# Optimization experiments

Measured on AMD Instinct MI355X. Metric: run time of the kernel, lower is better.

The kernel has to match this reference:

```python
import jax, jax.numpy as jnp
import numpy as np

L = 10                      # layers
DIL = [2 ** l for l in range(L)]  # dilations, kernel_size = 2
C = 128                     # residual channels
CS = 256                    # skip channels
V = 256                     # q_levels / vocab
B = 32                      # batch of decode streams
RF = 1 + sum(DIL)           # receptive field = 1024


def setup_inputs() -> dict:
    key = jax.random.key(0)
    ks = jax.random.split(key, 16)
    s = 1.0 / np.sqrt(C)
    inp = {
        "prompt": jax.random.randint(ks[0], (B, RF), 0, V, dtype=jnp.int32),
        "n_steps": 512,
        "E": jax.random.normal(ks[1], (V, C), jnp.float32) * 0.1,
        "Wf": jax.random.normal(ks[2], (L, C, C, 2), jnp.float32) * s,
        "Wg": jax.random.normal(ks[3], (L, C, C, 2), jnp.float32) * s,
        "bf": jnp.zeros((L, C), jnp.float32),
        "bg": jnp.zeros((L, C), jnp.float32),
        "Wres": jax.random.normal(ks[4], (L, C, C), jnp.float32) * s,
        "bres": jnp.zeros((L, C), jnp.float32),
        "Wskip": jax.random.normal(ks[5], (L, C, CS), jnp.float32) * s,
        "bskip": jnp.zeros((L, CS), jnp.float32),
        "Wo1": jax.random.normal(ks[6], (CS, CS), jnp.float32) / np.sqrt(CS),
        "bo1": jnp.zeros((CS,), jnp.float32),
        "Wo2": jax.random.normal(ks[7], (CS, V), jnp.float32) / np.sqrt(CS),
        "bo2": jnp.zeros((V,), jnp.float32),
    }
    return inp


def reference(prompt, n_steps, E, Wf, Wg, bf, bg, Wres, bres,
              Wskip, bskip, Wo1, bo1, Wo2, bo2):
    # ---- teacher-forced pass over the prompt: fills per-layer queues ----
    def head(skips):
        h = jax.nn.relu(skips)
        h = jax.nn.relu(h @ Wo1 + bo1)
        return h @ Wo2 + bo2

    x = E[prompt]                              # [B, T, C]
    skips = jnp.zeros((), jnp.float32)
    layer_ins = []                             # input to each residual layer
    T = prompt.shape[1]
    for l, d in enumerate(DIL):
        layer_ins.append(x)
        xd = jnp.pad(x, ((0, 0), (d, 0), (0, 0)))[:, :T]   # causal shift by d
        f = jnp.tanh(xd @ Wf[l, ..., 0] + x @ Wf[l, ..., 1] + bf[l])
        g = jax.nn.sigmoid(xd @ Wg[l, ..., 0] + x @ Wg[l, ..., 1] + bg[l])
        z = f * g
        skips = skips + z @ Wskip[l] + bskip[l]
        x = x + z @ Wres[l] + bres[l]
    logits = head(skips)                       # [B, T, V]
    tok0 = jnp.argmax(logits[:, -1], axis=-1).astype(prompt.dtype)  # first prediction
    # per-layer rolling queue: last d_l inputs to layer l (ring buffer)
    bufs = tuple(layer_ins[l][:, -DIL[l]:, :] for l in range(L))

    # ---- single-sample decode loop (rolling-queue fast generation) ----
    def step(carry, _):
        tok, bufs = carry
        x = E[tok]                             # [B, C]
        skips = jnp.zeros((), jnp.float32)
        new_bufs = []
        for l in range(L):
            past = bufs[l][:, 0, :]            # x_{t - d_l}
            f = jnp.tanh(past @ Wf[l, ..., 0] + x @ Wf[l, ..., 1] + bf[l])
            g = jax.nn.sigmoid(past @ Wg[l, ..., 0] + x @ Wg[l, ..., 1] + bg[l])
            z = f * g
            skips = skips + z @ Wskip[l] + bskip[l]
            # roll queue and push this layer's current input
            new_bufs.append(jnp.roll(bufs[l], -1, axis=1).at[:, -1, :].set(x))
            x = x + z @ Wres[l] + bres[l]
        nxt = jnp.argmax(head(skips), axis=-1).astype(tok.dtype)
        return (nxt, tuple(new_bufs)), tok

    (_, _), toks = jax.lax.scan(step, (tok0, bufs), None, length=n_steps)
    return jnp.concatenate([prompt, toks.T], axis=1)   # [B, T + n_steps]
```

## Files before the change

### kernel.cpp

```cpp
#include <hip/hip_runtime.h>
#include <math.h>

#define NL 10
#define C 128
#define CS 256
#define NV 256
#define NB 32
#define TT 1024
#define WPC 8
#define NTHR 256
#define CH_STRIDE 8192

__device__ __forceinline__ float atomLoadF(const float* p) {
  return __hip_atomic_load(p, __ATOMIC_RELAXED, __HIP_MEMORY_SCOPE_AGENT);
}
__device__ __forceinline__ void atomStoreF(float* p, float v) {
  __hip_atomic_store(p, v, __ATOMIC_RELAXED, __HIP_MEMORY_SCOPE_AGENT);
}
__device__ __forceinline__ unsigned atomLoadU(const unsigned* p) {
  return __hip_atomic_load(p, __ATOMIC_RELAXED, __HIP_MEMORY_SCOPE_AGENT);
}
__device__ __forceinline__ void atomStoreU(unsigned* p, unsigned v) {
  __hip_atomic_store(p, v, __ATOMIC_RELAXED, __HIP_MEMORY_SCOPE_AGENT);
}

__device__ __forceinline__ void chainbar(unsigned* ctr, unsigned& target) {
  target += WPC;
  asm volatile("s_waitcnt vmcnt(0) lgkmcnt(0)" ::: "memory");
  __syncthreads();
  if (threadIdx.x == 0) {
    __hip_atomic_fetch_add(ctr, 1u, __ATOMIC_RELAXED, __HIP_MEMORY_SCOPE_AGENT);
    while (__hip_atomic_load(ctr, __ATOMIC_RELAXED, __HIP_MEMORY_SCOPE_AGENT) < target) {}
  }
  __syncthreads();
  asm volatile("" ::: "memory");
}

__global__ __launch_bounds__(256) void k_embed(const int* __restrict__ prompt,
                                               const float* __restrict__ E,
                                               float* __restrict__ X) {
  int idx = blockIdx.x * 256 + threadIdx.x;
  const float4* E4 = (const float4*)E;
  float4* X4 = (float4*)X;
#pragma unroll
  for (int p = 0; p < 4; ++p) {
    int i = idx + p * 262144;
    int row = i >> 5, c4 = i & 31;
    int tk = prompt[row];
    X4[i] = E4[tk * 32 + c4];
  }
}

__global__ __launch_bounds__(256) void k_layer(
    const float* __restrict__ Xin, float* __restrict__ Xout,
    const float* __restrict__ Wf, const float* __restrict__ Wg,
    const float* __restrict__ bf, const float* __restrict__ bg,
    const float* __restrict__ Wres, const float* __restrict__ bres,
    float* __restrict__ rings, float* __restrict__ zlast, int l) {
  const int tid = threadIdx.x;
  const int m = blockIdx.x;
  const int b = m >> 3;
  const int t0 = (m & 7) << 7;
  const int d = 1 << l;

  __shared__ __align__(16) float sm[12416];
  float* Axd = sm;
  float* Ax  = sm + 16 * 132;
  float* Wfs = sm + 32 * 132;
  float* Wgs = Wfs + 16 * 256;

  const int rg = tid >> 4, cg = tid & 15;

  float af[8][8] = {};
  float ag[8][8] = {};

  for (int kc = 0; kc < 8; ++kc) {
    __syncthreads();
#pragma unroll
    for (int p = 0; p < 2; ++p) {
      int li = tid + p * 256;
      int row = li >> 2, c4 = li & 3;
      int ci = kc * 16 + c4 * 4;
      int t = t0 + row;
      float4 vx = *(const float4*)(Xin + ((size_t)b * TT + t) * C + ci);
      float4 vd = make_float4(0.f, 0.f, 0.f, 0.f);
      int ts = t - d;
      if (ts >= 0) vd = *(const float4*)(Xin + ((size_t)b * TT + ts) * C + ci);
      Ax[(c4 * 4 + 0) * 132 + row] = vx.x;
      Ax[(c4 * 4 + 1) * 132 + row] = vx.y;
      Ax[(c4 * 4 + 2) * 132 + row] = vx.z;
      Ax[(c4 * 4 + 3) * 132 + row] = vx.w;
      Axd[(c4 * 4 + 0) * 132 + row] = vd.x;
      Axd[(c4 * 4 + 1) * 132 + row] = vd.y;
      Axd[(c4 * 4 + 2) * 132 + row] = vd.z;
      Axd[(c4 * 4 + 3) * 132 + row] = vd.w;
    }
#pragma unroll
    for (int p = 0; p < 4; ++p) {
      int li = tid + p * 256;
      int ci = li >> 6, cc = (li & 63) << 2;
      size_t off = ((size_t)(l * C + kc * 16 + ci) * C) * 2 + cc;
      *(float4*)&Wfs[ci * 256 + cc] = *(const float4*)(Wf + off);
      *(float4*)&Wgs[ci * 256 + cc] = *(const float4*)(Wg + off);
    }
    __syncthreads();
    for (int ci = 0; ci < 16; ++ci) {
      float4 d0 = *(float4*)&Axd[ci * 132 + rg * 8];
      float4 d1 = *(float4*)&Axd[ci * 132 + rg * 8 + 4];
      float4 x0 = *(float4*)&Ax[ci * 132 + rg * 8];
      float4 x1 = *(float4*)&Ax[ci * 132 + rg * 8 + 4];
      float axd[8] = {d0.x, d0.y, d0.z, d0.w, d1.x, d1.y, d1.z, d1.w};
      float ax[8]  = {x0.x, x0.y, x0.z, x0.w, x1.x, x1.y, x1.z, x1.w};
#pragma unroll
      for (int jj = 0; jj < 4; ++jj) {
        float4 wf = *(float4*)&Wfs[ci * 256 + cg * 16 + jj * 4];
        float4 wg = *(float4*)&Wgs[ci * 256 + cg * 16 + jj * 4];
#pragma unroll
        for (int i = 0; i < 8; ++i) {
          af[i][2 * jj]     += axd[i] * wf.x + ax[i] * wf.y;
          af[i][2 * jj + 1] += axd[i] * wf.z + ax[i] * wf.w;
          ag[i][2 * jj]     += axd[i] * wg.x + ax[i] * wg.y;
          ag[i][2 * jj + 1] += axd[i] * wg.z + ax[i] * wg.w;
        }
      }
    }
  }

  float bfv[8], bgv[8];
#pragma unroll
  for (int j = 0; j < 8; ++j) {
    bfv[j] = bf[l * C + cg * 8 + j];
    bgv[j] = bg[l * C + cg * 8 + j];
  }
#pragma unroll
  for (int i = 0; i < 8; ++i)
#pragma unroll
    for (int j = 0; j < 8; ++j) {
      float fv = tanhf(af[i][j] + bfv[j]);
      float gv = 1.f / (1.f + expf(-(ag[i][j] + bgv[j])));
      af[i][j] = fv * gv;
    }
  if (((m & 7) == 7) && rg == 15) {
#pragma unroll
    for (int j = 0; j < 8; ++j)
      zlast[((size_t)l * NB + b) * C + cg * 8 + j] = af[7][j];
  }
#pragma unroll
  for (int i = 0; i < 8; ++i)
#pragma unroll
    for (int j = 0; j < 8; ++j) ag[i][j] = 0.f;

  float* zs  = sm;
  float* Wrs = sm + 32 * 132;
  for (int c = 0; c < 4; ++c) {
    __syncthreads();
    if ((cg >> 2) == c) {
      int kl = (cg & 3) * 8;
#pragma unroll
      for (int i = 0; i < 8; ++i)
#pragma unroll
        for (int j = 0; j < 8; ++j) zs[(kl + j) * 132 + rg * 8 + i] = af[i][j];
    }
#pragma unroll
    for (int p = 0; p < 4; ++p) {
      int li = tid + p * 256;
      int kr = li >> 5, cc = (li & 31) << 2;
      *(float4*)&Wrs[kr * 128 + cc] =
          *(const float4*)(Wres + ((size_t)(l * C + c * 32 + kr)) * C + cc);
    }
    __syncthreads();
    for (int k = 0; k < 32; ++k) {
      float4 a0 = *(float4*)&zs[k * 132 + rg * 8];
      float4 a1 = *(float4*)&zs[k * 132 + rg * 8 + 4];
      float4 w0 = *(float4*)&Wrs[k * 128 + cg * 8];
      float4 w1 = *(float4*)&Wrs[k * 128 + cg * 8 + 4];
      float a[8] = {a0.x, a0.y, a0.z, a0.w, a1.x, a1.y, a1.z, a1.w};
      float wv[8] = {w0.x, w0.y, w0.z, w0.w, w1.x, w1.y, w1.z, w1.w};
#pragma unroll
      for (int i = 0; i < 8; ++i)
#pragma unroll
        for (int j = 0; j < 8; ++j) ag[i][j] += a[i] * wv[j];
    }
  }

  float brv[8];
#pragma unroll
  for (int j = 0; j < 8; ++j) brv[j] = bres[l * C + cg * 8 + j];
#pragma unroll
  for (int i = 0; i < 8; ++i) {
    int t = t0 + rg * 8 + i;
    const float4* xi = (const float4*)(Xin + ((size_t)b * TT + t) * C + cg * 8);
    float4 v0 = xi[0], v1 = xi[1];
    float o[8] = {v0.x, v0.y, v0.z, v0.w, v1.x, v1.y, v1.z, v1.w};
#pragma unroll
    for (int j = 0; j < 8; ++j) o[j] += brv[j] + ag[i][j];
    float4* xo = (float4*)(Xout + ((size_t)b * TT + t) * C + cg * 8);
    xo[0] = make_float4(o[0], o[1], o[2], o[3]);
    xo[1] = make_float4(o[4], o[5], o[6], o[7]);
    if (t >= TT - d) {
      int slot = t - (TT - d);
      float* rp = rings + (size_t)(d - 1) * NB * C + ((size_t)slot * NB + b) * C + cg * 8;
      *(float4*)&rp[0] = v0;
      *(float4*)&rp[4] = v1;
    }
  }
}

__global__ __launch_bounds__(256) void k_head0(
    const float* __restrict__ zlast, const float* __restrict__ Wskip,
    const float* __restrict__ bskip, const float* __restrict__ Wo1,
    const float* __restrict__ bo1, const float* __restrict__ Wo2,
    const float* __restrict__ bo2, float* __restrict__ chst,
    int* __restrict__ dout, int ostride) {
  int b = blockIdx.x, tid = threadIdx.x;
  __shared__ float zl[NL][C];
  __shared__ float sr[CS];
  __shared__ float h1[CS];
  __shared__ float lg[NV];
#pragma unroll
  for (int p = 0; p < 5; ++p) {
    int li = tid + p * 256;
    zl[li >> 7][li & 127] = zlast[((size_t)(li >> 7) * NB + b) * C + (li & 127)];
  }
  __syncthreads();
  float s = 0.f;
  for (int l = 0; l < NL; ++l) {
    s += bskip[l * CS + tid];
    const float* wp = Wskip + (size_t)(l * C) * CS + tid;
    for (int k = 0; k < C; ++k) s += zl[l][k] * wp[(size_t)k * CS];
  }
  sr[tid] = fmaxf(s, 0.f);
  __syncthreads();
  float h = bo1[tid];
  {
    const float* wp = Wo1 + tid;
    for (int k = 0; k < CS; ++k) h += sr[k] * wp[(size_t)k * CS];
  }
  h1[tid] = fmaxf(h, 0.f);
  __syncthreads();
  float lv = bo2[tid];
  {
    const float* wp = Wo2 + tid;
    for (int k = 0; k < CS; ++k) lv += h1[k] * wp[(size_t)k * NV];
  }
  lg[tid] = lv;
  __syncthreads();
  if (tid == 0) {
    float bv = lg[0]; int bi = 0;
    for (int v = 1; v < NV; ++v)
      if (lg[v] > bv) { bv = lg[v]; bi = v; }
    ((unsigned*)(chst + (size_t)b * CH_STRIDE))[16] = (unsigned)bi;
    dout[(size_t)b * ostride + TT] = bi;
  }
}

__global__ __launch_bounds__(256) void k_copyprompt(const int* __restrict__ prompt,
                                                    int* __restrict__ dout,
                                                    int ostride) {
  int idx = blockIdx.x * 256 + threadIdx.x;
  int b = idx >> 10, t = idx & 1023;
  dout[(size_t)b * ostride + t] = prompt[idx];
}

__global__ __launch_bounds__(NTHR) void k_decode(
    const float* __restrict__ E, const float* __restrict__ Wf,
    const float* __restrict__ Wg, const float* __restrict__ bf,
    const float* __restrict__ bg, const float* __restrict__ Wres,
    const float* __restrict__ bres, const float* __restrict__ Wskip,
    const float* __restrict__ bskip, const float* __restrict__ Wo1,
    const float* __restrict__ bo1, const float* __restrict__ Wo2,
    const float* __restrict__ bo2, float* __restrict__ rings,
    float* __restrict__ chst, int* __restrict__ dout, int ostride) {
  const int tid = threadIdx.x;
  const int chain = blockIdx.x & 31;
  const int w = blockIdx.x >> 5;
  const int nsteps = ostride - TT;

  float* st = chst + (size_t)chain * CH_STRIDE;
  unsigned* ctr = (unsigned*)st;
  float* xpart = st + 64;
  float* skipp = st + 2176;
  float* h1g   = st + 4224;
  float* pmaxg = st + 4480;
  unsigned* pidxg = (unsigned*)(st + 4488);

  __shared__ float past[NL][C];
  __shared__ float xx[C];
  __shared__ float zbuf[16];
  __shared__ float fred[16][17];
  __shared__ float gred[16][17];
  __shared__ float skipr[CS];
  __shared__ float h1f[CS];
  __shared__ float hred[32][9];
  __shared__ float lgt[32];
  __shared__ float bsum[CS];
  __shared__ unsigned toksh;

  {
    float s = 0.f;
    for (int l = 0; l < NL; ++l) s += bskip[l * CS + tid];
    bsum[tid] = s;
  }
  __syncthreads();
  unsigned tok = ((const unsigned*)st)[16];
  unsigned target = 0;

  const int col = tid & 15, kg = tid >> 4;
  const int hj = tid & 31, hkg = tid >> 5;

  for (int s = 0; s < nsteps - 1; ++s) {
    if (tid < C) xx[tid] = E[(size_t)tok * C + tid];
#pragma unroll
    for (int p = 0; p < 5; ++p) {
      int li = tid + p * NTHR;
      int lp = li >> 7, cc = li & 127;
      int dd = 1 << lp;
      int slot = s & (dd - 1);
      past[lp][cc] = atomLoadF(
          &rings[(size_t)(dd - 1) * NB * C + (size_t)slot * NB * C + chain * C + cc]);
    }
    float skip_acc = 0.f;
    __syncthreads();

    for (int l = 0; l < NL; ++l) {
      const float* wfp = Wf + ((size_t)(l * C) * C + (w * 16 + col)) * 2;
      const float* wgp = Wg + ((size_t)(l * C) * C + (w * 16 + col)) * 2;
      float pf = 0.f, pg = 0.f;
#pragma unroll
      for (int i = 0; i < 8; ++i) {
        int ci = kg + 16 * i;
        float2 wf2 = *(const float2*)(wfp + (size_t)ci * C * 2);
        float2 wg2 = *(const float2*)(wgp + (size_t)ci * C * 2);
        float pv = past[l][ci], xv = xx[ci];
        pf += pv * wf2.x + xv * wf2.y;
        pg += pv * wg2.x + xv * wg2.y;
      }
      fred[col][kg] = pf;
      gred[col][kg] = pg;
      __syncthreads();
      if (tid < 16) {
        float sf = 0.f, sg = 0.f;
#pragma unroll
        for (int k = 0; k < 16; ++k) { sf += fred[tid][k]; sg += gred[tid][k]; }
        sf += bf[l * C + w * 16 + tid];
        sg += bg[l * C + w * 16 + tid];
        zbuf[tid] = tanhf(sf) * (1.f / (1.f + expf(-sg)));
      }
      __syncthreads();
      {
        const float* wsp = Wskip + (size_t)(l * C + w * 16) * CS + tid;
        float a = 0.f;
#pragma unroll
        for (int j = 0; j < 16; ++j) a += zbuf[j] * wsp[(size_t)j * CS];
        skip_acc += a;
      }
      if (l < NL - 1) {
        float oldx = 0.f;
        if (tid < C) {
          const float* wrp = Wres + (size_t)(l * C + w * 16) * C + tid;
          float a = 0.f;
#pragma unroll
          for (int j = 0; j < 16; ++j) a += zbuf[j] * wrp[(size_t)j * C];
          atomStoreF(&xpart[((l & 1) * 8 + w) * C + tid], a);
          oldx = xx[tid];
        }
        chainbar(ctr, target);
        if (tid < C) {
          float nx = xx[tid] + bres[l * C + tid];
#pragma unroll
          for (int wi = 0; wi < 8; ++wi)
            nx += atomLoadF(&xpart[((l & 1) * 8 + wi) * C + tid]);
          if (w == 0) {
            int dd = 1 << l, slot = s & (dd - 1);
            atomStoreF(&rings[(size_t)(dd - 1) * NB * C + (size_t)slot * NB * C +
                              chain * C + tid],
                       oldx);
          }
          xx[tid] = nx;
        }
        __syncthreads();
      } else {
        if (w == 0 && tid < C) {
          int dd = 1 << l, slot = s & (dd - 1);
          atomStoreF(&rings[(size_t)(dd - 1) * NB * C + (size_t)slot * NB * C +
                            chain * C + tid],
                     xx[tid]);
        }
      }
    }

    atomStoreF(&skipp[w * CS + tid], skip_acc);
    chainbar(ctr, target);
    {
      float sk = bsum[tid];
#pragma unroll
      for (int wi = 0; wi < 8; ++wi) sk += atomLoadF(&skipp[wi * CS + tid]);
      skipr[tid] = fmaxf(sk, 0.f);
    }
    __syncthreads();
    {
      const float* wp = Wo1 + w * 32 + hj;
      float a = 0.f;
      for (int k = hkg * 32; k < hkg * 32 + 32; ++k) a += skipr[k] * wp[(size_t)k * CS];
      hred[hj][hkg] = a;
      __syncthreads();
      if (tid < 32) {
        float v = 0.f;
#pragma unroll
        for (int k = 0; k < 8; ++k) v += hred[tid][k];
        v += bo1[w * 32 + tid];
        atomStoreF(&h1g[w * 32 + tid], fmaxf(v, 0.f));
      }
    }
    chainbar(ctr, target);
    h1f[tid] = atomLoadF(&h1g[tid]);
    __syncthreads();
    {
      const float* wp = Wo2 + w * 32 + hj;
      float a = 0.f;
      for (int k = hkg * 32; k < hkg * 32 + 32; ++k) a += h1f[k] * wp[(size_t)k * NV];
      hred[hj][hkg] = a;
      __syncthreads();
      if (tid < 32) {
        float v = 0.f;
#pragma unroll
        for (int k = 0; k < 8; ++k) v += hred[tid][k];
        lgt[tid] = v + bo2[w * 32 + tid];
      }
      __syncthreads();
      if (tid == 0) {
        float bv = lgt[0]; int bi = 0;
        for (int j = 1; j < 32; ++j)
          if (lgt[j] > bv) { bv = lgt[j]; bi = j; }
        atomStoreF(&pmaxg[w], bv);
        atomStoreU(&pidxg[w], (unsigned)(w * 32 + bi));
      }
    }
    chainbar(ctr, target);
    if (tid == 0) {
      float bv = atomLoadF(&pmaxg[0]);
      unsigned bi = atomLoadU(&pidxg[0]);
#pragma unroll
      for (int wi = 1; wi < 8; ++wi) {
        float v = atomLoadF(&pmaxg[wi]);
        if (v > bv) { bv = v; bi = atomLoadU(&pidxg[wi]); }
      }
      toksh = bi;
      if (w == 0) dout[(size_t)chain * ostride + TT + s + 1] = (int)bi;
    }
    __syncthreads();
    tok = toksh;
  }
}

extern "C" void kernel_launch(void* const* d_in, const int* in_sizes, int n_in,
                              void* d_out, int out_size, void* d_ws, size_t ws_size,
                              hipStream_t stream) {
  const int* prompt = (const int*)d_in[0];
  const float* E    = (const float*)d_in[2];
  const float* Wf   = (const float*)d_in[3];
  const float* Wg   = (const float*)d_in[4];
  const float* bf   = (const float*)d_in[5];
  const float* bg   = (const float*)d_in[6];
  const float* Wres = (const float*)d_in[7];
  const float* bres = (const float*)d_in[8];
  const float* Wskip= (const float*)d_in[9];
  const float* bskip= (const float*)d_in[10];
  const float* Wo1  = (const float*)d_in[11];
  const float* bo1  = (const float*)d_in[12];
  const float* Wo2  = (const float*)d_in[13];
  const float* bo2  = (const float*)d_in[14];
  int* dout = (int*)d_out;
  int ostride = out_size / NB;

  float* ws = (float*)d_ws;
  float* X0    = ws;
  float* X1    = ws + 4194304;
  float* rings = ws + 8388608;
  float* zlast = ws + 12578816;
  float* chst  = ws + 12619776;

  hipMemsetAsync(chst, 0, (size_t)NB * CH_STRIDE * sizeof(float), stream);
  k_embed<<<1024, 256, 0, stream>>>(prompt, E, X0);
  float* xa = X0; float* xb = X1;
  for (int l = 0; l < NL; ++l) {
    k_layer<<<256, 256, 0, stream>>>(xa, xb, Wf, Wg, bf, bg, Wres, bres, rings, zlast, l);
    float* t = xa; xa = xb; xb = t;
  }
  k_head0<<<NB, 256, 0, stream>>>(zlast, Wskip, bskip, Wo1, bo1, Wo2, bo2, chst, dout, ostride);
  k_copyprompt<<<128, 256, 0, stream>>>(prompt, dout, ostride);
  k_decode<<<NB * WPC, NTHR, 0, stream>>>(E, Wf, Wg, bf, bg, Wres, bres, Wskip, bskip,
                                          Wo1, bo1, Wo2, bo2, rings, chst, dout, ostride);
}
```

Baseline: 35.18 ms.

## Replace counter barriers with tagged 64-bit flag exchange and register weight prefetch

Cross-block synchronisation in the decode loop stops using a shared atomic counter barrier. Each value now travels as a 64-bit word holding a float and a step tag, and consumers spin until the tags match. Gate, skip, residual and head weights are prefetched into registers one layer ahead, and the past-input half of the gate dot product is computed early. The ring buffer is filled for the next step while the skip reduction is still pending, and biases are cached in shared memory. Storage for rings and exchange buffers doubles, register pressure rises, and per-slot tag spinning adds polling traffic.

```diff
diff --git a/kernel.cpp b/kernel.cpp
--- a/kernel.cpp
+++ b/kernel.cpp
@@ -9,31 +9,21 @@
 #define TT 1024
 #define WPC 8
 #define NTHR 256
-#define CH_STRIDE 8192
-
-__device__ __forceinline__ float atomLoadF(const float* p) {
+#define CH_BYTES 131072
+
+typedef unsigned long long ull;
+
+__device__ __forceinline__ ull aLoad64(const ull* p) {
   return __hip_atomic_load(p, __ATOMIC_RELAXED, __HIP_MEMORY_SCOPE_AGENT);
 }
-__device__ __forceinline__ void atomStoreF(float* p, float v) {
+__device__ __forceinline__ void aStore64(ull* p, ull v) {
   __hip_atomic_store(p, v, __ATOMIC_RELAXED, __HIP_MEMORY_SCOPE_AGENT);
 }
-__device__ __forceinline__ unsigned atomLoadU(const unsigned* p) {
-  return __hip_atomic_load(p, __ATOMIC_RELAXED, __HIP_MEMORY_SCOPE_AGENT);
-}
-__device__ __forceinline__ void atomStoreU(unsigned* p, unsigned v) {
-  __hip_atomic_store(p, v, __ATOMIC_RELAXED, __HIP_MEMORY_SCOPE_AGENT);
-}
-
-__device__ __forceinline__ void chainbar(unsigned* ctr, unsigned& target) {
-  target += WPC;
-  asm volatile("s_waitcnt vmcnt(0) lgkmcnt(0)" ::: "memory");
-  __syncthreads();
-  if (threadIdx.x == 0) {
-    __hip_atomic_fetch_add(ctr, 1u, __ATOMIC_RELAXED, __HIP_MEMORY_SCOPE_AGENT);
-    while (__hip_atomic_load(ctr, __ATOMIC_RELAXED, __HIP_MEMORY_SCOPE_AGENT) < target) {}
-  }
-  __syncthreads();
-  asm volatile("" ::: "memory");
+__device__ __forceinline__ ull packF(float x, unsigned tag) {
+  return ((ull)__float_as_uint(x) << 32) | (ull)tag;
+}
+__device__ __forceinline__ float unpackF(ull v) {
+  return __uint_as_float((unsigned)(v >> 32));
 }
 
 __global__ __launch_bounds__(256) void k_embed(const int* __restrict__ prompt,
@@ -56,7 +46,7 @@
     const float* __restrict__ Wf, const float* __restrict__ Wg,
     const float* __restrict__ bf, const float* __restrict__ bg,
     const float* __restrict__ Wres, const float* __restrict__ bres,
-    float* __restrict__ rings, float* __restrict__ zlast, int l) {
+    ull* __restrict__ rings, float* __restrict__ zlast, int l) {
   const int tid = threadIdx.x;
   const int m = blockIdx.x;
   const int b = m >> 3;
@@ -199,9 +189,10 @@
     xo[1] = make_float4(o[4], o[5], o[6], o[7]);
     if (t >= TT - d) {
       int slot = t - (TT - d);
-      float* rp = rings + (size_t)(d - 1) * NB * C + ((size_t)slot * NB + b) * C + cg * 8;
-      *(float4*)&rp[0] = v0;
-      *(float4*)&rp[4] = v1;
+      ull* rp = rings + (size_t)(d - 1) * NB * C + ((size_t)slot * NB + b) * C + cg * 8;
+      float vin[8] = {v0.x, v0.y, v0.z, v0.w, v1.x, v1.y, v1.z, v1.w};
+#pragma unroll
+      for (int j = 0; j < 8; ++j) rp[j] = packF(vin[j], 0u);
     }
   }
 }
@@ -210,7 +201,7 @@
     const float* __restrict__ zlast, const float* __restrict__ Wskip,
     const float* __restrict__ bskip, const float* __restrict__ Wo1,
     const float* __restrict__ bo1, const float* __restrict__ Wo2,
-    const float* __restrict__ bo2, float* __restrict__ chst,
+    const float* __restrict__ bo2, char* __restrict__ chst,
     int* __restrict__ dout, int ostride) {
   int b = blockIdx.x, tid = threadIdx.x;
   __shared__ float zl[NL][C];
@@ -249,7 +240,7 @@
     float bv = lg[0]; int bi = 0;
     for (int v = 1; v < NV; ++v)
       if (lg[v] > bv) { bv = lg[v]; bi = v; }
-    ((unsigned*)(chst + (size_t)b * CH_STRIDE))[16] = (unsigned)bi;
+    *(unsigned*)(chst + (size_t)b * CH_BYTES) = (unsigned)bi;
     dout[(size_t)b * ostride + TT] = bi;
   }
 }
@@ -262,78 +253,128 @@
   dout[(size_t)b * ostride + t] = prompt[idx];
 }
 
-__global__ __launch_bounds__(NTHR) void k_decode(
+__global__ __launch_bounds__(NTHR, 1) void k_decode(
     const float* __restrict__ E, const float* __restrict__ Wf,
     const float* __restrict__ Wg, const float* __restrict__ bf,
     const float* __restrict__ bg, const float* __restrict__ Wres,
     const float* __restrict__ bres, const float* __restrict__ Wskip,
     const float* __restrict__ bskip, const float* __restrict__ Wo1,
     const float* __restrict__ bo1, const float* __restrict__ Wo2,
-    const float* __restrict__ bo2, float* __restrict__ rings,
-    float* __restrict__ chst, int* __restrict__ dout, int ostride) {
+    const float* __restrict__ bo2, ull* __restrict__ rings,
+    char* __restrict__ chst, int* __restrict__ dout, int ostride) {
   const int tid = threadIdx.x;
   const int chain = blockIdx.x & 31;
   const int w = blockIdx.x >> 5;
   const int nsteps = ostride - TT;
 
-  float* st = chst + (size_t)chain * CH_STRIDE;
-  unsigned* ctr = (unsigned*)st;
-  float* xpart = st + 64;
-  float* skipp = st + 2176;
-  float* h1g   = st + 4224;
-  float* pmaxg = st + 4480;
-  unsigned* pidxg = (unsigned*)(st + 4488);
+  char* cb = chst + (size_t)chain * CH_BYTES;
+  ull* xp  = (ull*)(cb + 1024);
+  ull* skp = (ull*)(cb + 74752);
+  ull* h1p = (ull*)(cb + 91136);
+  ull* amx = (ull*)(cb + 93184);
 
   __shared__ float past[NL][C];
   __shared__ float xx[C];
-  __shared__ float zbuf[16];
   __shared__ float fred[16][17];
   __shared__ float gred[16][17];
+  __shared__ float zbuf[16];
   __shared__ float skipr[CS];
   __shared__ float h1f[CS];
   __shared__ float hred[32][9];
   __shared__ float lgt[32];
+  __shared__ ull am[8];
+  __shared__ float bfl[NL][16], bgl[NL][16];
+  __shared__ float brl[NL - 1][C];
   __shared__ float bsum[CS];
-  __shared__ unsigned toksh;
-
+
+  for (int li = tid; li < NL * 16; li += NTHR) {
+    bfl[li >> 4][li & 15] = bf[(li >> 4) * C + w * 16 + (li & 15)];
+    bgl[li >> 4][li & 15] = bg[(li >> 4) * C + w * 16 + (li & 15)];
+  }
+  for (int li = tid; li < (NL - 1) * C; li += NTHR)
+    brl[li >> 7][li & 127] = bres[(li >> 7) * C + (li & 127)];
   {
-    float s = 0.f;
-    for (int l = 0; l < NL; ++l) s += bskip[l * CS + tid];
-    bsum[tid] = s;
-  }
-  __syncthreads();
-  unsigned tok = ((const unsigned*)st)[16];
-  unsigned target = 0;
+    float sacc = 0.f;
+    for (int l = 0; l < NL; ++l) sacc += bskip[l * CS + tid];
+    bsum[tid] = sacc;
+  }
+
+  unsigned tok = *(const unsigned*)cb;
 
   const int col = tid & 15, kg = tid >> 4;
   const int hj = tid & 31, hkg = tid >> 5;
 
-  for (int s = 0; s < nsteps - 1; ++s) {
-    if (tid < C) xx[tid] = E[(size_t)tok * C + tid];
+  float2 gwf[2][8], gwg[2][8];
+  float wresr[2][16], wskipr[2][16];
+  float pfp[2], pgp[2];
+
+  auto ringLoad = [&](int s2) {
 #pragma unroll
     for (int p = 0; p < 5; ++p) {
       int li = tid + p * NTHR;
       int lp = li >> 7, cc = li & 127;
-      int dd = 1 << lp;
-      int slot = s & (dd - 1);
-      past[lp][cc] = atomLoadF(
-          &rings[(size_t)(dd - 1) * NB * C + (size_t)slot * NB * C + chain * C + cc]);
+      int D = 1 << lp;
+      int slot = s2 & (D - 1);
+      unsigned expv = (s2 >= D) ? (unsigned)(s2 - D + 1) : 0u;
+      const ull* rp =
+          rings + (size_t)(D - 1) * NB * C + ((size_t)slot * NB + chain) * C + cc;
+      ull v = aLoad64(rp);
+      while ((unsigned)v != expv) v = aLoad64(rp);
+      past[lp][cc] = unpackF(v);
+    }
+  };
+  auto gatePrefetch = [&](int l, int buf) {
+#pragma unroll
+    for (int i = 0; i < 8; ++i) {
+      int ci = kg + 16 * i;
+      gwf[buf][i] = *(const float2*)(Wf + ((size_t)(l * C + ci) * C + (w * 16 + col)) * 2);
+      gwg[buf][i] = *(const float2*)(Wg + ((size_t)(l * C + ci) * C + (w * 16 + col)) * 2);
+    }
+#pragma unroll
+    for (int j = 0; j < 16; ++j)
+      wskipr[buf][j] = Wskip[(size_t)(l * C + w * 16 + j) * CS + tid];
+    if (l < NL - 1 && tid < C) {
+#pragma unroll
+      for (int j = 0; j < 16; ++j)
+        wresr[buf][j] = Wres[(size_t)(l * C + w * 16 + j) * C + tid];
+    }
+  };
+  auto pastDot = [&](int l, int buf) {
+    float a = 0.f, bacc = 0.f;
+#pragma unroll
+    for (int i = 0; i < 8; ++i) {
+      float pv = past[l][kg + 16 * i];
+      a += pv * gwf[buf][i].x;
+      bacc += pv * gwg[buf][i].x;
+    }
+    pfp[buf] = a;
+    pgp[buf] = bacc;
+  };
+
+  ringLoad(0);
+  gatePrefetch(0, 0);
+  __syncthreads();
+  pastDot(0, 0);
+
+  for (int s = 0; s < nsteps - 1; ++s) {
+    const unsigned tg = (unsigned)(s + 1);
+    float xreg = 0.f;
+    if (tid < C) {
+      xreg = E[(size_t)tok * C + tid];
+      xx[tid] = xreg;
     }
     float skip_acc = 0.f;
     __syncthreads();
 
+#pragma unroll
     for (int l = 0; l < NL; ++l) {
-      const float* wfp = Wf + ((size_t)(l * C) * C + (w * 16 + col)) * 2;
-      const float* wgp = Wg + ((size_t)(l * C) * C + (w * 16 + col)) * 2;
-      float pf = 0.f, pg = 0.f;
+      const int buf = l & 1, nbuf = buf ^ 1;
+      float pf = pfp[buf], pg = pgp[buf];
 #pragma unroll
       for (int i = 0; i < 8; ++i) {
-        int ci = kg + 16 * i;
-        float2 wf2 = *(const float2*)(wfp + (size_t)ci * C * 2);
-        float2 wg2 = *(const float2*)(wgp + (size_t)ci * C * 2);
-        float pv = past[l][ci], xv = xx[ci];
-        pf += pv * wf2.x + xv * wf2.y;
-        pg += pv * wg2.x + xv * wg2.y;
+        float xv = xx[kg + 16 * i];
+        pf += xv * gwf[buf][i].y;
+        pg += xv * gwg[buf][i].y;
       }
       fred[col][kg] = pf;
       gred[col][kg] = pg;
@@ -342,114 +383,155 @@
         float sf = 0.f, sg = 0.f;
 #pragma unroll
         for (int k = 0; k < 16; ++k) { sf += fred[tid][k]; sg += gred[tid][k]; }
-        sf += bf[l * C + w * 16 + tid];
-        sg += bg[l * C + w * 16 + tid];
-        zbuf[tid] = tanhf(sf) * (1.f / (1.f + expf(-sg)));
+        sf += bfl[l][tid];
+        sg += bgl[l][tid];
+        zbuf[tid] = tanhf(sf) / (1.f + expf(-sg));
       }
       __syncthreads();
-      {
-        const float* wsp = Wskip + (size_t)(l * C + w * 16) * CS + tid;
-        float a = 0.f;
-#pragma unroll
-        for (int j = 0; j < 16; ++j) a += zbuf[j] * wsp[(size_t)j * CS];
-        skip_acc += a;
-      }
+      float oldx = xreg;
       if (l < NL - 1) {
-        float oldx = 0.f;
         if (tid < C) {
-          const float* wrp = Wres + (size_t)(l * C + w * 16) * C + tid;
-          float a = 0.f;
-#pragma unroll
-          for (int j = 0; j < 16; ++j) a += zbuf[j] * wrp[(size_t)j * C];
-          atomStoreF(&xpart[((l & 1) * 8 + w) * C + tid], a);
-          oldx = xx[tid];
+          float part = 0.f;
+#pragma unroll
+          for (int j = 0; j < 16; ++j) part += zbuf[j] * wresr[buf][j];
+          aStore64(&xp[((size_t)l * 8 + w) * C + tid], packF(part, tg));
         }
-        chainbar(ctr, target);
+        gatePrefetch(l + 1, nbuf);
+        {
+          float sa = 0.f;
+#pragma unroll
+          for (int j = 0; j < 16; ++j) sa += zbuf[j] * wskipr[buf][j];
+          skip_acc += sa;
+        }
+        pastDot(l + 1, nbuf);
         if (tid < C) {
-          float nx = xx[tid] + bres[l * C + tid];
-#pragma unroll
-          for (int wi = 0; wi < 8; ++wi)
-            nx += atomLoadF(&xpart[((l & 1) * 8 + wi) * C + tid]);
-          if (w == 0) {
-            int dd = 1 << l, slot = s & (dd - 1);
-            atomStoreF(&rings[(size_t)(dd - 1) * NB * C + (size_t)slot * NB * C +
-                              chain * C + tid],
-                       oldx);
+          const ull* base = &xp[(size_t)l * 8 * C + tid];
+          ull v[8];
+          bool ok;
+          do {
+            ok = true;
+#pragma unroll
+            for (int i2 = 0; i2 < 8; ++i2) v[i2] = aLoad64(base + (size_t)i2 * C);
+#pragma unroll
+            for (int i2 = 0; i2 < 8; ++i2) ok &= ((unsigned)v[i2] == tg);
+          } while (!ok);
+          float xnew = oldx + brl[l][tid];
+#pragma unroll
+          for (int i2 = 0; i2 < 8; ++i2) xnew += unpackF(v[i2]);
+          xreg = xnew;
+          xx[tid] = xnew;
+          if (w == (l & 7)) {
+            int D = 1 << l, slot = s & (D - 1);
+            aStore64(&rings[(size_t)(D - 1) * NB * C + ((size_t)slot * NB + chain) * C + tid],
+                     packF(oldx, tg));
           }
-          xx[tid] = nx;
         }
         __syncthreads();
       } else {
-        if (w == 0 && tid < C) {
-          int dd = 1 << l, slot = s & (dd - 1);
-          atomStoreF(&rings[(size_t)(dd - 1) * NB * C + (size_t)slot * NB * C +
-                            chain * C + tid],
-                     xx[tid]);
+        {
+          float sa = 0.f;
+#pragma unroll
+          for (int j = 0; j < 16; ++j) sa += zbuf[j] * wskipr[buf][j];
+          skip_acc += sa;
+        }
+        if (w == (9 & 7) && tid < C) {
+          int slot = s & 511;
+          aStore64(&rings[(size_t)511 * NB * C + ((size_t)slot * NB + chain) * C + tid],
+                   packF(xreg, tg));
         }
       }
     }
 
-    atomStoreF(&skipp[w * CS + tid], skip_acc);
-    chainbar(ctr, target);
+    aStore64(&skp[(size_t)w * CS + tid], packF(skip_acc, tg));
+    gatePrefetch(0, 0);
+    float wo1r[32];
+#pragma unroll
+    for (int k2 = 0; k2 < 32; ++k2)
+      wo1r[k2] = Wo1[(size_t)(hkg * 32 + k2) * CS + w * 32 + hj];
+    ringLoad(s + 1);
     {
+      const ull* base = &skp[tid];
+      ull v[8];
+      bool ok;
+      do {
+        ok = true;
+#pragma unroll
+        for (int i2 = 0; i2 < 8; ++i2) v[i2] = aLoad64(base + (size_t)i2 * CS);
+#pragma unroll
+        for (int i2 = 0; i2 < 8; ++i2) ok &= ((unsigned)v[i2] == tg);
+      } while (!ok);
       float sk = bsum[tid];
 #pragma unroll
-      for (int wi = 0; wi < 8; ++wi) sk += atomLoadF(&skipp[wi * CS + tid]);
+      for (int i2 = 0; i2 < 8; ++i2) sk += unpackF(v[i2]);
       skipr[tid] = fmaxf(sk, 0.f);
     }
     __syncthreads();
+    pastDot(0, 0);
     {
-      const float* wp = Wo1 + w * 32 + hj;
       float a = 0.f;
-      for (int k = hkg * 32; k < hkg * 32 + 32; ++k) a += skipr[k] * wp[(size_t)k * CS];
+#pragma unroll
+      for (int k2 = 0; k2 < 32; ++k2) a += skipr[hkg * 32 + k2] * wo1r[k2];
       hred[hj][hkg] = a;
-      __syncthreads();
-      if (tid < 32) {
-        float v = 0.f;
-#pragma unroll
-        for (int k = 0; k < 8; ++k) v += hred[tid][k];
-        v += bo1[w * 32 + tid];
-        atomStoreF(&h1g[w * 32 + tid], fmaxf(v, 0.f));
+    }
+    __syncthreads();
+    if (tid < 32) {
+      float v2 = 0.f;
+#pragma unroll
+      for (int k2 = 0; k2 < 8; ++k2) v2 += hred[tid][k2];
+      v2 += bo1[w * 32 + tid];
+      aStore64(&h1p[(size_t)w * 32 + tid], packF(fmaxf(v2, 0.f), tg));
+    }
+    float wo2r[32];
+#pragma unroll
+    for (int k2 = 0; k2 < 32; ++k2)
+      wo2r[k2] = Wo2[(size_t)(hkg * 32 + k2) * NV + w * 32 + hj];
+    {
+      ull v2 = aLoad64(&h1p[tid]);
+      while ((unsigned)v2 != tg) v2 = aLoad64(&h1p[tid]);
+      h1f[tid] = unpackF(v2);
+    }
+    __syncthreads();
+    {
+      float a = 0.f;
+#pragma unroll
+      for (int k2 = 0; k2 < 32; ++k2) a += h1f[hkg * 32 + k2] * wo2r[k2];
+      hred[hj][hkg] = a;
+    }
+    __syncthreads();
+    if (tid < 32) {
+      float v2 = 0.f;
+#pragma unroll
+      for (int k2 = 0; k2 < 8; ++k2) v2 += hred[tid][k2];
+      lgt[tid] = v2 + bo2[w * 32 + tid];
+    }
+    __syncthreads();
+    if (tid == 0) {
+      float bv = lgt[0];
+      int bi = 0;
+#pragma unroll
+      for (int j = 1; j < 32; ++j)
+        if (lgt[j] > bv) { bv = lgt[j]; bi = j; }
+      ull pv = ((ull)__float_as_uint(bv) << 32) | ((ull)tg << 8) | (unsigned)(w * 32 + bi);
+      aStore64(&amx[w], pv);
+    }
+    if (tid < 8) {
+      ull v2 = aLoad64(&amx[tid]);
+      while ((unsigned)((v2 >> 8) & 0xFFFFFF) != tg) v2 = aLoad64(&amx[tid]);
+      am[tid] = v2;
+    }
+    __syncthreads();
+    {
+      float bv = unpackF(am[0]);
+      unsigned bi = (unsigned)(am[0] & 255);
+#pragma unroll
+      for (int i2 = 1; i2 < 8; ++i2) {
+        float v2 = unpackF(am[i2]);
+        if (v2 > bv) { bv = v2; bi = (unsigned)(am[i2] & 255); }
       }
-    }
-    chainbar(ctr, target);
-    h1f[tid] = atomLoadF(&h1g[tid]);
-    __syncthreads();
-    {
-      const float* wp = Wo2 + w * 32 + hj;
-      float a = 0.f;
-      for (int k = hkg * 32; k < hkg * 32 + 32; ++k) a += h1f[k] * wp[(size_t)k * NV];
-      hred[hj][hkg] = a;
-      __syncthreads();
-      if (tid < 32) {
-        float v = 0.f;
-#pragma unroll
-        for (int k = 0; k < 8; ++k) v += hred[tid][k];
-        lgt[tid] = v + bo2[w * 32 + tid];
-      }
-      __syncthreads();
-      if (tid == 0) {
-        float bv = lgt[0]; int bi = 0;
-        for (int j = 1; j < 32; ++j)
-          if (lgt[j] > bv) { bv = lgt[j]; bi = j; }
-        atomStoreF(&pmaxg[w], bv);
-        atomStoreU(&pidxg[w], (unsigned)(w * 32 + bi));
-      }
-    }
-    chainbar(ctr, target);
-    if (tid == 0) {
-      float bv = atomLoadF(&pmaxg[0]);
-      unsigned bi = atomLoadU(&pidxg[0]);
-#pragma unroll
-      for (int wi = 1; wi < 8; ++wi) {
-        float v = atomLoadF(&pmaxg[wi]);
-        if (v > bv) { bv = v; bi = atomLoadU(&pidxg[wi]); }
-      }
-      toksh = bi;
-      if (w == 0) dout[(size_t)chain * ostride + TT + s + 1] = (int)bi;
-    }
-    __syncthreads();
-    tok = toksh;
+      tok = bi;
+      if (w == 0 && tid == 0) dout[(size_t)chain * ostride + TT + s + 1] = (int)bi;
+    }
+    __syncthreads();
   }
 }
 
@@ -473,16 +555,16 @@
   int* dout = (int*)d_out;
   int ostride = out_size / NB;
 
-  float* ws = (float*)d_ws;
-  float* X0    = ws;
-  float* X1    = ws + 4194304;
-  float* rings = ws + 8388608;
-  float* zlast = ws + 12578816;
-  float* chst  = ws + 12619776;
-
-  hipMemsetAsync(chst, 0, (size_t)NB * CH_STRIDE * sizeof(float), stream);
+  char* ws = (char*)d_ws;
+  float* X0   = (float*)ws;
+  float* X1   = (float*)(ws + 16777216);
+  ull* rings  = (ull*)(ws + 33554432);
+  float* zlast= (float*)(ws + 67076096);
+  char* chst  = ws + 67239936;
+
   k_embed<<<1024, 256, 0, stream>>>(prompt, E, X0);
-  float* xa = X0; float* xb = X1;
+  float* xa = X0;
+  float* xb = X1;
   for (int l = 0; l < NL; ++l) {
     k_layer<<<256, 256, 0, stream>>>(xa, xb, Wf, Wg, bf, bg, Wres, bres, rings, zlast, l);
     float* t = xa; xa = xb; xb = t;
```

New measurement: 88.74 ms. +152.2%, slower.
